# Performance work log

Hardware: AMD Instinct MI355X
Metric: run time of the kernel (lower is better)

The kernel has to match this reference:

```python
import jax, jax.numpy as jnp
import numpy as np


def setup_inputs() -> dict:
    key = jax.random.key(0)
    ks = jax.random.split(key, 5)
    S, B, E, H = 512, 64, 1024, 1024
    scale = 0.02
    return {
        "x": jax.random.normal(ks[0], (S, B, E), dtype=jnp.float32),
        "W_all": jax.random.normal(ks[1], (4 * H, E + H), dtype=jnp.float32) * scale,
        "b_all": jnp.zeros((4 * H,), dtype=jnp.float32),
        "Q": jax.random.normal(ks[2], (E, H), dtype=jnp.float32) * scale,
        "R": jax.random.normal(ks[3], (H, E), dtype=jnp.float32) * scale,
        "mog_iters": 5,
    }


def reference(x, W_all, b_all, Q, R, mog_iters):
    # x: [S, B, E] (length-first). Returns (outputs [S,B,H], (ht, ct)).
    S, B, E = x.shape
    H = W_all.shape[0] // 4

    def step(carry, xt):
        ht, ct = carry
        # Mogrifier rounds (odd rounds update x, even rounds update h)
        for i in range(1, mog_iters + 1):
            if i % 2:
                xt = 2.0 * jax.nn.sigmoid(ht @ Q.T) * xt
            else:
                ht = 2.0 * jax.nn.sigmoid(xt @ R.T) * ht
        z = jnp.concatenate([xt, ht], axis=-1) @ W_all.T + b_all  # [B, 4H]
        i_g, f_g, g_g, o_g = jnp.split(z, 4, axis=-1)
        ct = jax.nn.sigmoid(f_g) * ct + jax.nn.sigmoid(i_g) * jnp.tanh(g_g)
        ht = jax.nn.sigmoid(o_g) * jnp.tanh(ct)
        return (ht, ct), ht

    h0 = jnp.zeros((B, H), dtype=x.dtype)
    c0 = jnp.zeros((B, H), dtype=x.dtype)
    (ht, ct), outputs = jax.lax.scan(step, (h0, c0), x)
    return outputs, (ht, ct)
```

## Files before the change

### kernel.cpp

```cpp
#include <hip/hip_runtime.h>
#include <hip/hip_bf16.h>
#include <math.h>


using bf16   = __bf16;
using bf16x4 = __attribute__((ext_vector_type(4))) __bf16;
using bf16x8 = __attribute__((ext_vector_type(8))) __bf16;
using f32x4  = __attribute__((ext_vector_type(4))) float;

#define MFMA16(a,b,c) __builtin_amdgcn_mfma_f32_16x16x32_bf16((a),(b),(c),0,0,0)

__device__ __forceinline__ float fsig(float x) { return 1.f / (1.f + expf(-x)); }

__global__ void prep(const float* __restrict__ Q, const float* __restrict__ R,
                     const float* __restrict__ Wf,
                     bf16* __restrict__ Qh, bf16* __restrict__ Ql,
                     bf16* __restrict__ Rh, bf16* __restrict__ Rl,
                     bf16* __restrict__ Whi, bf16* __restrict__ Wlo,
                     float* __restrict__ hM, float* __restrict__ cM,
                     bf16* __restrict__ Nh, bf16* __restrict__ Nl, int wsplit) {
  const long tid = (long)blockIdx.x * blockDim.x + threadIdx.x;
  const long nth = (long)gridDim.x * blockDim.x;
  for (long i = tid; i < 1024L * 1024 / 4; i += nth) {
    float4 v = ((const float4*)Q)[i];
    bf16 a0 = (bf16)v.x, a1 = (bf16)v.y, a2 = (bf16)v.z, a3 = (bf16)v.w;
    Qh[i*4+0] = a0; Qh[i*4+1] = a1; Qh[i*4+2] = a2; Qh[i*4+3] = a3;
    Ql[i*4+0] = (bf16)(v.x - (float)a0); Ql[i*4+1] = (bf16)(v.y - (float)a1);
    Ql[i*4+2] = (bf16)(v.z - (float)a2); Ql[i*4+3] = (bf16)(v.w - (float)a3);
    float4 u = ((const float4*)R)[i];
    bf16 b0 = (bf16)u.x, b1 = (bf16)u.y, b2 = (bf16)u.z, b3 = (bf16)u.w;
    Rh[i*4+0] = b0; Rh[i*4+1] = b1; Rh[i*4+2] = b2; Rh[i*4+3] = b3;
    Rl[i*4+0] = (bf16)(u.x - (float)b0); Rl[i*4+1] = (bf16)(u.y - (float)b1);
    Rl[i*4+2] = (bf16)(u.z - (float)b2); Rl[i*4+3] = (bf16)(u.w - (float)b3);
  }
  if (wsplit) {
    for (long i = tid; i < 4096L * 2048 / 4; i += nth) {
      float4 v = ((const float4*)Wf)[i];
      bf16 a0 = (bf16)v.x, a1 = (bf16)v.y, a2 = (bf16)v.z, a3 = (bf16)v.w;
      Whi[i*4+0] = a0; Whi[i*4+1] = a1; Whi[i*4+2] = a2; Whi[i*4+3] = a3;
      Wlo[i*4+0] = (bf16)(v.x - (float)a0); Wlo[i*4+1] = (bf16)(v.y - (float)a1);
      Wlo[i*4+2] = (bf16)(v.z - (float)a2); Wlo[i*4+3] = (bf16)(v.w - (float)a3);
    }
  }
  for (long i = tid; i < 64L * 1024; i += nth) {
    hM[i] = 0.f; cM[i] = 0.f; Nh[i] = (bf16)0.f; Nl[i] = (bf16)0.f;
  }
}

__global__ __launch_bounds__(512) void mog_phase(
    const bf16* __restrict__ Ah, const bf16* __restrict__ Al,
    const bf16* __restrict__ Bh, const bf16* __restrict__ Bl,
    const float* __restrict__ mult, float* __restrict__ dstM,
    bf16* __restrict__ Dh, bf16* __restrict__ Dl) {
  __shared__ f32x4 red[7][64];
  const int mt = blockIdx.x >> 6, c = blockIdx.x & 63;
  const int tid = threadIdx.x, l = tid & 63, w = tid >> 6;
  const int r16 = l & 15, kg = l >> 4;
  const size_t kb = (size_t)w * 128 + kg * 8;
  const bf16* bhp = Bh + (size_t)(16 * c + r16) * 1024 + kb;
  const bf16* blp = Bl + (size_t)(16 * c + r16) * 1024 + kb;
  const bf16* ahp = Ah + (size_t)(16 * mt + r16) * 1024 + kb;
  const bf16* alp = Al + (size_t)(16 * mt + r16) * 1024 + kb;
  f32x4 acc = {};
#pragma unroll
  for (int ks = 0; ks < 4; ++ks) {
    bf16x8 bh = *(const bf16x8*)(bhp + ks * 32);
    bf16x8 bl = *(const bf16x8*)(blp + ks * 32);
    bf16x8 ah = *(const bf16x8*)(ahp + ks * 32);
    bf16x8 al = *(const bf16x8*)(alp + ks * 32);
    acc = MFMA16(al, bl, acc);
    acc = MFMA16(al, bh, acc);
    acc = MFMA16(ah, bl, acc);
    acc = MFMA16(ah, bh, acc);
  }
  if (w) red[w - 1][l] = acc;
  __syncthreads();
  if (w == 0) {
#pragma unroll
    for (int kk = 0; kk < 7; ++kk) acc += red[kk][l];
    const int col = 16 * c + r16;
#pragma unroll
    for (int q = 0; q < 4; ++q) {
      const int row = 16 * mt + kg * 4 + q;
      const size_t idx = (size_t)row * 1024 + col;
      float v = 2.f * fsig(acc[q]) * mult[idx];
      dstM[idx] = v;
      bf16 hi = (bf16)v;
      Dh[idx] = hi;
      Dl[idx] = (bf16)(v - (float)hi);
    }
  }
}

template <int WSPLIT>
__global__ __launch_bounds__(512) void gate4(
    const bf16* __restrict__ Xh, const bf16* __restrict__ Xl,
    const bf16* __restrict__ Hh, const bf16* __restrict__ Hl,
    const float* __restrict__ Wf, const bf16* __restrict__ Whi,
    const bf16* __restrict__ Wlo, const float* __restrict__ ball,
    float* __restrict__ cM, float* __restrict__ hM,
    bf16* __restrict__ Nh, bf16* __restrict__ Nl,
    float* __restrict__ out, int t) {
  __shared__ f32x4 red[8][4][64];
  const int g = blockIdx.x;
  const int tid = threadIdx.x, l = tid & 63, w = tid >> 6;
  const int r16 = l & 15, kg = l >> 4;
  const bf16* Abh = (w < 4) ? Xh : Hh;
  const bf16* Abl = (w < 4) ? Xl : Hl;
  const size_t kb = (size_t)(w & 3) * 256 + kg * 8;
  const size_t wrow = (size_t)(r16 >> 2) * 1024 + 4 * g + (r16 & 3);
  const float* wp  = Wf  + wrow * 2048 + (size_t)w * 256 + kg * 8;
  const bf16*  whp = Whi + wrow * 2048 + (size_t)w * 256 + kg * 8;
  const bf16*  wlp = Wlo + wrow * 2048 + (size_t)w * 256 + kg * 8;
  f32x4 acc[4] = {};
#pragma unroll
  for (int ks = 0; ks < 8; ++ks) {
    bf16x8 bh, bl;
    if (WSPLIT) {
      bh = *(const bf16x8*)(whp + ks * 32);
      bl = *(const bf16x8*)(wlp + ks * 32);
    } else {
      f32x4 w0 = *(const f32x4*)(wp + ks * 32);
      f32x4 w1 = *(const f32x4*)(wp + ks * 32 + 4);
#pragma unroll
      for (int e = 0; e < 4; ++e) {
        bf16 t0 = (bf16)w0[e]; bh[e] = t0;     bl[e] = (bf16)(w0[e] - (float)t0);
        bf16 t1 = (bf16)w1[e]; bh[4 + e] = t1; bl[4 + e] = (bf16)(w1[e] - (float)t1);
      }
    }
#pragma unroll
    for (int m = 0; m < 4; ++m) {
      bf16x8 ah = *(const bf16x8*)(Abh + (size_t)(16 * m + r16) * 1024 + kb + ks * 32);
      bf16x8 al = *(const bf16x8*)(Abl + (size_t)(16 * m + r16) * 1024 + kb + ks * 32);
      acc[m] = MFMA16(al, bl, acc[m]);
      acc[m] = MFMA16(al, bh, acc[m]);
      acc[m] = MFMA16(ah, bl, acc[m]);
      acc[m] = MFMA16(ah, bh, acc[m]);
    }
  }
#pragma unroll
  for (int m = 0; m < 4; ++m) red[w][m][l] = acc[m];
  __syncthreads();
  if (tid < 256) {
    const int row = tid >> 2, hc = tid & 3;
    const int m = row >> 4, rem = row & 15;
    const int kgq = rem >> 2, q = rem & 3;
    const int hcg = 4 * g + hc;
    float z[4];
#pragma unroll
    for (int gg = 0; gg < 4; ++gg) {
      const int lane = kgq * 16 + gg * 4 + hc;
      float s = red[0][m][lane][q];
#pragma unroll
      for (int kk = 1; kk < 8; ++kk) s += red[kk][m][lane][q];
      z[gg] = s;
    }
    const float zi = z[0] + ball[hcg];
    const float zf = z[1] + ball[1024 + hcg];
    const float zg = z[2] + ball[2048 + hcg];
    const float zo = z[3] + ball[3072 + hcg];
    const size_t idx = (size_t)row * 1024 + hcg;
    const float cc = fsig(zf) * cM[idx] + fsig(zi) * tanhf(zg);
    const float hh = fsig(zo) * tanhf(cc);
    cM[idx] = cc;
    hM[idx] = hh;
    bf16 hib = (bf16)hh;
    Nh[idx] = hib;
    Nl[idx] = (bf16)(hh - (float)hib);
    out[(size_t)t * 65536 + idx] = hh;
    if (t == 511) {
      out[(size_t)512 * 65536 + idx] = hh;
      out[(size_t)512 * 65536 + 65536 + idx] = cc;
    }
  }
}

extern "C" void kernel_launch(void* const* d_in, const int* in_sizes, int n_in,
                              void* d_out, int out_size, void* d_ws, size_t ws_size,
                              hipStream_t stream) {
  (void)in_sizes; (void)n_in; (void)out_size;
  const float* x    = (const float*)d_in[0];
  const float* Wall = (const float*)d_in[1];
  const float* ball = (const float*)d_in[2];
  const float* Q    = (const float*)d_in[3];
  const float* R    = (const float*)d_in[4];
  float* out = (float*)d_out;

  char* ws = (char*)d_ws;
  size_t off = 0;
  bf16* Qh = (bf16*)(ws + off); off += (size_t)1024 * 1024 * 2;
  bf16* Ql = (bf16*)(ws + off); off += (size_t)1024 * 1024 * 2;
  bf16* Rh = (bf16*)(ws + off); off += (size_t)1024 * 1024 * 2;
  bf16* Rl = (bf16*)(ws + off); off += (size_t)1024 * 1024 * 2;
  bf16* Xh = (bf16*)(ws + off); off += (size_t)64 * 1024 * 2;
  bf16* Xl = (bf16*)(ws + off); off += (size_t)64 * 1024 * 2;
  bf16* Hh = (bf16*)(ws + off); off += (size_t)64 * 1024 * 2;
  bf16* Hl = (bf16*)(ws + off); off += (size_t)64 * 1024 * 2;
  bf16* Nh = (bf16*)(ws + off); off += (size_t)64 * 1024 * 2;
  bf16* Nl = (bf16*)(ws + off); off += (size_t)64 * 1024 * 2;
  float* xM = (float*)(ws + off); off += (size_t)64 * 1024 * 4;
  float* hM = (float*)(ws + off); off += (size_t)64 * 1024 * 4;
  float* cM = (float*)(ws + off); off += (size_t)64 * 1024 * 4;
  bf16* Whi = (bf16*)(ws + off);
  bf16* Wlo = (bf16*)(ws + off + (size_t)4096 * 2048 * 2);
  const int wsplit = (ws_size >= off + (size_t)2 * 4096 * 2048 * 2) ? 1 : 0;

  prep<<<512, 256, 0, stream>>>(Q, R, Wall, Qh, Ql, Rh, Rl, Whi, Wlo,
                                hM, cM, Nh, Nl, wsplit);
  for (int t = 0; t < 512; ++t) {
    const float* xt = x + (size_t)t * 65536;
    mog_phase<<<256, 512, 0, stream>>>(Nh, Nl, Qh, Ql, xt, xM, Xh, Xl);
    mog_phase<<<256, 512, 0, stream>>>(Xh, Xl, Rh, Rl, hM, hM, Hh, Hl);
    mog_phase<<<256, 512, 0, stream>>>(Hh, Hl, Qh, Ql, xM, xM, Xh, Xl);
    mog_phase<<<256, 512, 0, stream>>>(Xh, Xl, Rh, Rl, hM, hM, Hh, Hl);
    mog_phase<<<256, 512, 0, stream>>>(Hh, Hl, Qh, Ql, xM, xM, Xh, Xl);
    if (wsplit)
      gate4<1><<<256, 512, 0, stream>>>(Xh, Xl, Hh, Hl, Wall, Whi, Wlo, ball,
                                        cM, hM, Nh, Nl, out, t);
    else
      gate4<0><<<256, 512, 0, stream>>>(Xh, Xl, Hh, Hl, Wall, Whi, Wlo, ball,
                                        cM, hM, Nh, Nl, out, t);
  }
}
```

Measured before the change: 27.96 ms.

## Overlap h-half of gate GEMM with fifth mogrifier round, widen blocks to 1024 threads

The fifth mogrifier round now shares a launch with the h-part of the gate matmul, since that part depends only on the final h. Partial gate sums go to a workspace buffer, and the final kernel adds the x-part and applies the LSTM cell. All kernels move to 1024-thread blocks with 16-way K splits. The pre-split bf16 copy of W is dropped, so W is converted from fp32 inside the kernel at every step. This trades extra conversion work and a zbuf round trip for more parallelism and a shorter dependency chain.

```diff
diff --git a/kernel.cpp b/kernel.cpp
--- a/kernel.cpp
+++ b/kernel.cpp
@@ -4,7 +4,6 @@
 
 
 using bf16   = __bf16;
-using bf16x4 = __attribute__((ext_vector_type(4))) __bf16;
 using bf16x8 = __attribute__((ext_vector_type(8))) __bf16;
 using f32x4  = __attribute__((ext_vector_type(4))) float;
 
@@ -13,12 +12,10 @@
 __device__ __forceinline__ float fsig(float x) { return 1.f / (1.f + expf(-x)); }
 
 __global__ void prep(const float* __restrict__ Q, const float* __restrict__ R,
-                     const float* __restrict__ Wf,
                      bf16* __restrict__ Qh, bf16* __restrict__ Ql,
                      bf16* __restrict__ Rh, bf16* __restrict__ Rl,
-                     bf16* __restrict__ Whi, bf16* __restrict__ Wlo,
                      float* __restrict__ hM, float* __restrict__ cM,
-                     bf16* __restrict__ Nh, bf16* __restrict__ Nl, int wsplit) {
+                     bf16* __restrict__ Nh, bf16* __restrict__ Nl) {
   const long tid = (long)blockIdx.x * blockDim.x + threadIdx.x;
   const long nth = (long)gridDim.x * blockDim.x;
   for (long i = tid; i < 1024L * 1024 / 4; i += nth) {
@@ -33,37 +30,28 @@
     Rl[i*4+0] = (bf16)(u.x - (float)b0); Rl[i*4+1] = (bf16)(u.y - (float)b1);
     Rl[i*4+2] = (bf16)(u.z - (float)b2); Rl[i*4+3] = (bf16)(u.w - (float)b3);
   }
-  if (wsplit) {
-    for (long i = tid; i < 4096L * 2048 / 4; i += nth) {
-      float4 v = ((const float4*)Wf)[i];
-      bf16 a0 = (bf16)v.x, a1 = (bf16)v.y, a2 = (bf16)v.z, a3 = (bf16)v.w;
-      Whi[i*4+0] = a0; Whi[i*4+1] = a1; Whi[i*4+2] = a2; Whi[i*4+3] = a3;
-      Wlo[i*4+0] = (bf16)(v.x - (float)a0); Wlo[i*4+1] = (bf16)(v.y - (float)a1);
-      Wlo[i*4+2] = (bf16)(v.z - (float)a2); Wlo[i*4+3] = (bf16)(v.w - (float)a3);
-    }
-  }
   for (long i = tid; i < 64L * 1024; i += nth) {
     hM[i] = 0.f; cM[i] = 0.f; Nh[i] = (bf16)0.f; Nl[i] = (bf16)0.f;
   }
 }
 
-__global__ __launch_bounds__(512) void mog_phase(
+__device__ __forceinline__ void mog_body(
+    int mt, int c, int tid, char* smem,
     const bf16* __restrict__ Ah, const bf16* __restrict__ Al,
     const bf16* __restrict__ Bh, const bf16* __restrict__ Bl,
     const float* __restrict__ mult, float* __restrict__ dstM,
     bf16* __restrict__ Dh, bf16* __restrict__ Dl) {
-  __shared__ f32x4 red[7][64];
-  const int mt = blockIdx.x >> 6, c = blockIdx.x & 63;
-  const int tid = threadIdx.x, l = tid & 63, w = tid >> 6;
+  f32x4* red = (f32x4*)smem;
+  const int l = tid & 63, w = tid >> 6;
   const int r16 = l & 15, kg = l >> 4;
-  const size_t kb = (size_t)w * 128 + kg * 8;
+  const size_t kb = (size_t)w * 64 + kg * 8;
   const bf16* bhp = Bh + (size_t)(16 * c + r16) * 1024 + kb;
   const bf16* blp = Bl + (size_t)(16 * c + r16) * 1024 + kb;
   const bf16* ahp = Ah + (size_t)(16 * mt + r16) * 1024 + kb;
   const bf16* alp = Al + (size_t)(16 * mt + r16) * 1024 + kb;
   f32x4 acc = {};
 #pragma unroll
-  for (int ks = 0; ks < 4; ++ks) {
+  for (int ks = 0; ks < 2; ++ks) {
     bf16x8 bh = *(const bf16x8*)(bhp + ks * 32);
     bf16x8 bl = *(const bf16x8*)(blp + ks * 32);
     bf16x8 ah = *(const bf16x8*)(ahp + ks * 32);
@@ -73,11 +61,11 @@
     acc = MFMA16(ah, bl, acc);
     acc = MFMA16(ah, bh, acc);
   }
-  if (w) red[w - 1][l] = acc;
+  if (w) red[(w - 1) * 64 + l] = acc;
   __syncthreads();
   if (w == 0) {
 #pragma unroll
-    for (int kk = 0; kk < 7; ++kk) acc += red[kk][l];
+    for (int kk = 0; kk < 15; ++kk) acc += red[kk * 64 + l];
     const int col = 16 * c + r16;
 #pragma unroll
     for (int q = 0; q < 4; ++q) {
@@ -92,41 +80,35 @@
   }
 }
 
-template <int WSPLIT>
-__global__ __launch_bounds__(512) void gate4(
-    const bf16* __restrict__ Xh, const bf16* __restrict__ Xl,
-    const bf16* __restrict__ Hh, const bf16* __restrict__ Hl,
-    const float* __restrict__ Wf, const bf16* __restrict__ Whi,
-    const bf16* __restrict__ Wlo, const float* __restrict__ ball,
-    float* __restrict__ cM, float* __restrict__ hM,
-    bf16* __restrict__ Nh, bf16* __restrict__ Nl,
-    float* __restrict__ out, int t) {
-  __shared__ f32x4 red[8][4][64];
-  const int g = blockIdx.x;
-  const int tid = threadIdx.x, l = tid & 63, w = tid >> 6;
+__global__ __launch_bounds__(1024) void mog_phase(
+    const bf16* __restrict__ Ah, const bf16* __restrict__ Al,
+    const bf16* __restrict__ Bh, const bf16* __restrict__ Bl,
+    const float* __restrict__ mult, float* __restrict__ dstM,
+    bf16* __restrict__ Dh, bf16* __restrict__ Dl) {
+  __shared__ __align__(16) char smem[15 * 64 * 16];
+  mog_body(blockIdx.x >> 6, blockIdx.x & 63, threadIdx.x, smem,
+           Ah, Al, Bh, Bl, mult, dstM, Dh, Dl);
+}
+
+__device__ __forceinline__ void halfgate_body(
+    int g, int tid, f32x4* red,
+    const bf16* __restrict__ Abh, const bf16* __restrict__ Abl,
+    const float* __restrict__ Wf, int khalf) {
+  const int l = tid & 63, w = tid >> 6;
   const int r16 = l & 15, kg = l >> 4;
-  const bf16* Abh = (w < 4) ? Xh : Hh;
-  const bf16* Abl = (w < 4) ? Xl : Hl;
-  const size_t kb = (size_t)(w & 3) * 256 + kg * 8;
+  const size_t kb = (size_t)w * 64 + kg * 8;
   const size_t wrow = (size_t)(r16 >> 2) * 1024 + 4 * g + (r16 & 3);
-  const float* wp  = Wf  + wrow * 2048 + (size_t)w * 256 + kg * 8;
-  const bf16*  whp = Whi + wrow * 2048 + (size_t)w * 256 + kg * 8;
-  const bf16*  wlp = Wlo + wrow * 2048 + (size_t)w * 256 + kg * 8;
+  const float* wp = Wf + wrow * 2048 + (size_t)khalf * 1024 + kb;
   f32x4 acc[4] = {};
 #pragma unroll
-  for (int ks = 0; ks < 8; ++ks) {
+  for (int ks = 0; ks < 2; ++ks) {
+    f32x4 w0 = *(const f32x4*)(wp + ks * 32);
+    f32x4 w1 = *(const f32x4*)(wp + ks * 32 + 4);
     bf16x8 bh, bl;
-    if (WSPLIT) {
-      bh = *(const bf16x8*)(whp + ks * 32);
-      bl = *(const bf16x8*)(wlp + ks * 32);
-    } else {
-      f32x4 w0 = *(const f32x4*)(wp + ks * 32);
-      f32x4 w1 = *(const f32x4*)(wp + ks * 32 + 4);
-#pragma unroll
-      for (int e = 0; e < 4; ++e) {
-        bf16 t0 = (bf16)w0[e]; bh[e] = t0;     bl[e] = (bf16)(w0[e] - (float)t0);
-        bf16 t1 = (bf16)w1[e]; bh[4 + e] = t1; bl[4 + e] = (bf16)(w1[e] - (float)t1);
-      }
+#pragma unroll
+    for (int e = 0; e < 4; ++e) {
+      bf16 t0 = (bf16)w0[e]; bh[e] = t0;     bl[e] = (bf16)(w0[e] - (float)t0);
+      bf16 t1 = (bf16)w1[e]; bh[4 + e] = t1; bl[4 + e] = (bf16)(w1[e] - (float)t1);
     }
 #pragma unroll
     for (int m = 0; m < 4; ++m) {
@@ -139,8 +121,50 @@
     }
   }
 #pragma unroll
-  for (int m = 0; m < 4; ++m) red[w][m][l] = acc[m];
+  for (int m = 0; m < 4; ++m) red[(w * 4 + m) * 64 + l] = acc[m];
   __syncthreads();
+}
+
+__global__ __launch_bounds__(1024) void mog5_zh(
+    const bf16* __restrict__ Hh, const bf16* __restrict__ Hl,
+    const bf16* __restrict__ Qh, const bf16* __restrict__ Ql,
+    const float* __restrict__ xM, float* __restrict__ dstM,
+    bf16* __restrict__ Xh, bf16* __restrict__ Xl,
+    const float* __restrict__ Wf, float* __restrict__ zbuf) {
+  __shared__ __align__(16) char smem[16 * 4 * 64 * 16];
+  const int bid = blockIdx.x, tid = threadIdx.x;
+  if (bid < 256) {
+    mog_body(bid >> 6, bid & 63, tid, smem, Hh, Hl, Qh, Ql, xM, dstM, Xh, Xl);
+    return;
+  }
+  const int g = bid - 256;
+  f32x4* red = (f32x4*)smem;
+  halfgate_body(g, tid, red, Hh, Hl, Wf, 1);
+  if (tid < 256) {
+    const int row = tid >> 2, hc = tid & 3;
+    const int m = row >> 4, rem = row & 15;
+    const int kgq = rem >> 2, q = rem & 3;
+#pragma unroll
+    for (int gg = 0; gg < 4; ++gg) {
+      const int lane = kgq * 16 + gg * 4 + hc;
+      float s = red[(0 * 4 + m) * 64 + lane][q];
+#pragma unroll
+      for (int kk = 1; kk < 16; ++kk) s += red[(kk * 4 + m) * 64 + lane][q];
+      zbuf[(size_t)row * 4096 + gg * 1024 + 4 * g + hc] = s;
+    }
+  }
+}
+
+__global__ __launch_bounds__(1024) void gate_x(
+    const bf16* __restrict__ Xh, const bf16* __restrict__ Xl,
+    const float* __restrict__ Wf, const float* __restrict__ zbuf,
+    const float* __restrict__ ball, float* __restrict__ cM,
+    float* __restrict__ hM, bf16* __restrict__ Nh, bf16* __restrict__ Nl,
+    float* __restrict__ out, int t) {
+  __shared__ __align__(16) char smem[16 * 4 * 64 * 16];
+  const int g = blockIdx.x, tid = threadIdx.x;
+  f32x4* red = (f32x4*)smem;
+  halfgate_body(g, tid, red, Xh, Xl, Wf, 0);
   if (tid < 256) {
     const int row = tid >> 2, hc = tid & 3;
     const int m = row >> 4, rem = row & 15;
@@ -150,18 +174,14 @@
 #pragma unroll
     for (int gg = 0; gg < 4; ++gg) {
       const int lane = kgq * 16 + gg * 4 + hc;
-      float s = red[0][m][lane][q];
-#pragma unroll
-      for (int kk = 1; kk < 8; ++kk) s += red[kk][m][lane][q];
-      z[gg] = s;
-    }
-    const float zi = z[0] + ball[hcg];
-    const float zf = z[1] + ball[1024 + hcg];
-    const float zg = z[2] + ball[2048 + hcg];
-    const float zo = z[3] + ball[3072 + hcg];
+      float s = red[(0 * 4 + m) * 64 + lane][q];
+#pragma unroll
+      for (int kk = 1; kk < 16; ++kk) s += red[(kk * 4 + m) * 64 + lane][q];
+      z[gg] = s + zbuf[(size_t)row * 4096 + gg * 1024 + hcg] + ball[gg * 1024 + hcg];
+    }
     const size_t idx = (size_t)row * 1024 + hcg;
-    const float cc = fsig(zf) * cM[idx] + fsig(zi) * tanhf(zg);
-    const float hh = fsig(zo) * tanhf(cc);
+    const float cc = fsig(z[1]) * cM[idx] + fsig(z[0]) * tanhf(z[2]);
+    const float hh = fsig(z[3]) * tanhf(cc);
     cM[idx] = cc;
     hM[idx] = hh;
     bf16 hib = (bf16)hh;
@@ -178,7 +198,7 @@
 extern "C" void kernel_launch(void* const* d_in, const int* in_sizes, int n_in,
                               void* d_out, int out_size, void* d_ws, size_t ws_size,
                               hipStream_t stream) {
-  (void)in_sizes; (void)n_in; (void)out_size;
+  (void)in_sizes; (void)n_in; (void)out_size; (void)ws_size;
   const float* x    = (const float*)d_in[0];
   const float* Wall = (const float*)d_in[1];
   const float* ball = (const float*)d_in[2];
@@ -201,24 +221,18 @@
   float* xM = (float*)(ws + off); off += (size_t)64 * 1024 * 4;
   float* hM = (float*)(ws + off); off += (size_t)64 * 1024 * 4;
   float* cM = (float*)(ws + off); off += (size_t)64 * 1024 * 4;
-  bf16* Whi = (bf16*)(ws + off);
-  bf16* Wlo = (bf16*)(ws + off + (size_t)4096 * 2048 * 2);
-  const int wsplit = (ws_size >= off + (size_t)2 * 4096 * 2048 * 2) ? 1 : 0;
-
-  prep<<<512, 256, 0, stream>>>(Q, R, Wall, Qh, Ql, Rh, Rl, Whi, Wlo,
-                                hM, cM, Nh, Nl, wsplit);
+  float* zbuf = (float*)(ws + off); off += (size_t)64 * 4096 * 4;
+
+  prep<<<512, 256, 0, stream>>>(Q, R, Qh, Ql, Rh, Rl, hM, cM, Nh, Nl);
   for (int t = 0; t < 512; ++t) {
     const float* xt = x + (size_t)t * 65536;
-    mog_phase<<<256, 512, 0, stream>>>(Nh, Nl, Qh, Ql, xt, xM, Xh, Xl);
-    mog_phase<<<256, 512, 0, stream>>>(Xh, Xl, Rh, Rl, hM, hM, Hh, Hl);
-    mog_phase<<<256, 512, 0, stream>>>(Hh, Hl, Qh, Ql, xM, xM, Xh, Xl);
-    mog_phase<<<256, 512, 0, stream>>>(Xh, Xl, Rh, Rl, hM, hM, Hh, Hl);
-    mog_phase<<<256, 512, 0, stream>>>(Hh, Hl, Qh, Ql, xM, xM, Xh, Xl);
-    if (wsplit)
-      gate4<1><<<256, 512, 0, stream>>>(Xh, Xl, Hh, Hl, Wall, Whi, Wlo, ball,
-                                        cM, hM, Nh, Nl, out, t);
-    else
-      gate4<0><<<256, 512, 0, stream>>>(Xh, Xl, Hh, Hl, Wall, Whi, Wlo, ball,
-                                        cM, hM, Nh, Nl, out, t);
-  }
-}
+    mog_phase<<<256, 1024, 0, stream>>>(Nh, Nl, Qh, Ql, xt, xM, Xh, Xl);
+    mog_phase<<<256, 1024, 0, stream>>>(Xh, Xl, Rh, Rl, hM, hM, Hh, Hl);
+    mog_phase<<<256, 1024, 0, stream>>>(Hh, Hl, Qh, Ql, xM, xM, Xh, Xl);
+    mog_phase<<<256, 1024, 0, stream>>>(Xh, Xl, Rh, Rl, hM, hM, Hh, Hl);
+    mog5_zh<<<512, 1024, 0, stream>>>(Hh, Hl, Qh, Ql, xM, xM, Xh, Xl,
+                                      Wall, zbuf);
+    gate_x<<<256, 1024, 0, stream>>>(Xh, Xl, Wall, zbuf, ball, cM, hM,
+                                     Nh, Nl, out, t);
+  }
+}
```

After: 28.41 ms. Within noise of the previous version (+1.6%).
